# Optimization experiments

Hardware: AMD Instinct MI355X
Metric: run time of the kernel (lower is better)

## Reference

```python
import jax, jax.numpy as jnp
import numpy as np

N_NODES = 50000
N_EDGES = 600000
D = 128          # in = hidden = out (forced by residual adds)
HEADS = 4
HEAD_DIM = D // HEADS
EPS = 1e-5
NEG_SLOPE = 0.2  # PyG GATConv default


def setup_inputs() -> dict:
    key = jax.random.key(0)
    ks = jax.random.split(key, 12)
    s = 1.0 / np.sqrt(D)
    x = jax.random.normal(ks[0], (N_NODES, D), dtype=jnp.float32)
    edge_index = jax.random.randint(ks[1], (2, N_EDGES), 0, N_NODES, dtype=jnp.int32)
    # conv1: GATConv(D, D//heads, heads=heads)
    W1 = jax.random.normal(ks[2], (D, D), dtype=jnp.float32) * s
    a_src1 = jax.random.normal(ks[3], (HEADS, HEAD_DIM), dtype=jnp.float32) * s
    a_dst1 = jax.random.normal(ks[4], (HEADS, HEAD_DIM), dtype=jnp.float32) * s
    b1 = jnp.zeros((D,), dtype=jnp.float32)
    # conv2: GATConv(D, D, heads=1)
    W2 = jax.random.normal(ks[5], (D, D), dtype=jnp.float32) * s
    a_src2 = jax.random.normal(ks[6], (1, D), dtype=jnp.float32) * s
    a_dst2 = jax.random.normal(ks[7], (1, D), dtype=jnp.float32) * s
    b2 = jnp.zeros((D,), dtype=jnp.float32)
    # shared AddAndNorm BatchNorm1d params (same module used twice)
    bn_gamma = jnp.ones((D,), dtype=jnp.float32)
    bn_beta = jnp.zeros((D,), dtype=jnp.float32)
    return {"x": x, "edge_index": edge_index,
            "W1": W1, "a_src1": a_src1, "a_dst1": a_dst1, "b1": b1,
            "W2": W2, "a_src2": a_src2, "a_dst2": a_dst2, "b2": b2,
            "bn_gamma": bn_gamma, "bn_beta": bn_beta}


def _gat_conv(x, W, a_src, a_dst, b, src, dst, heads, head_dim):
    n = x.shape[0]
    h = (x @ W).reshape(n, heads, head_dim)                 # [N,H,C]
    e_src = jnp.einsum('nhc,hc->nh', h, a_src)              # [N,H]
    e_dst = jnp.einsum('nhc,hc->nh', h, a_dst)
    e = jax.nn.leaky_relu(e_src[src] + e_dst[dst], NEG_SLOPE)  # [E,H]
    # segment softmax over incoming edges per destination node
    m = jax.ops.segment_max(e, dst, num_segments=n)
    alpha = jnp.exp(e - m[dst])
    denom = jax.ops.segment_sum(alpha, dst, num_segments=n)
    alpha = alpha / denom[dst]
    out = jax.ops.segment_sum(alpha[:, :, None] * h[src], dst, num_segments=n)
    return out.reshape(n, heads * head_dim) + b


def _batch_norm(x, gamma, beta):
    mean = jnp.mean(x, axis=0)
    var = jnp.var(x, axis=0)
    return (x - mean) * jax.lax.rsqrt(var + EPS) * gamma + beta


def reference(x, edge_index, W1, a_src1, a_dst1, b1, W2, a_src2, a_dst2, b2,
              bn_gamma, bn_beta):
    n = x.shape[0]
    # PyG GATConv adds self loops by default
    loops = jnp.arange(n, dtype=edge_index.dtype)
    src = jnp.concatenate([edge_index[0], loops])
    dst = jnp.concatenate([edge_index[1], loops])

    res = x
    h = _gat_conv(x, W1, a_src1, a_dst1, b1, src, dst, HEADS, HEAD_DIM)
    h = _batch_norm(h + res, bn_gamma, bn_beta)   # dropout is identity (eval)
    h = jax.nn.relu(h)
    res = h
    h = _gat_conv(h, W2, a_src2, a_dst2, b2, src, dst, 1, D)
    h = _batch_norm(h + res, bn_gamma, bn_beta)
    return h
```

## Files before the change

kernel.cpp:

```cpp
#include <hip/hip_runtime.h>
#include <math.h>

#define NN 50000
#define NE 600000
#define ET (NE + NN)
#define D 128
#define EPSB 1e-5f
#define SLOPE 0.2f
#define XPITCH 136
#define SCB 196

typedef float f32x4 __attribute__((ext_vector_type(4)));
typedef short bf16x8 __attribute__((ext_vector_type(8)));

__device__ inline unsigned short bf16r(float f) {
    unsigned int u = __float_as_uint(f);
    unsigned int r = (u + 0x7fff + ((u >> 16) & 1)) >> 16;
    return (unsigned short)r;
}
__device__ inline float bflo(unsigned int u) { return __uint_as_float(u << 16); }
__device__ inline float bfhi(unsigned int u) { return __uint_as_float(u & 0xffff0000u); }

__global__ void hist_kernel(const int* __restrict__ ei, int* __restrict__ deg) {
    int e = blockIdx.x * blockDim.x + threadIdx.x;
    if (e >= ET) return;
    int dst = (e < NE) ? ei[NE + e] : (e - NE);
    atomicAdd(&deg[dst], 1);
}

__global__ __launch_bounds__(256) void scan_a_kernel(const int* __restrict__ deg,
                                                     int* __restrict__ tmp,
                                                     int* __restrict__ bsum) {
    __shared__ int sm[256];
    int t = threadIdx.x;
    int idx = blockIdx.x * 256 + t;
    int v = (idx < NN) ? deg[idx] : 0;
    sm[t] = v;
    __syncthreads();
    #pragma unroll
    for (int d = 1; d < 256; d <<= 1) {
        int add = (t >= d) ? sm[t - d] : 0;
        __syncthreads();
        sm[t] += add;
        __syncthreads();
    }
    if (idx < NN) tmp[idx] = sm[t];
    if (t == 255) bsum[blockIdx.x] = sm[255];
}

__global__ __launch_bounds__(256) void scan_b_kernel(const int* __restrict__ deg,
                                                     const int* __restrict__ tmp,
                                                     const int* __restrict__ bsum,
                                                     int* __restrict__ offs,
                                                     int* __restrict__ cur) {
    __shared__ int sm[256];
    int t = threadIdx.x;
    sm[t] = (t < SCB) ? bsum[t] : 0;
    __syncthreads();
    #pragma unroll
    for (int d = 1; d < 256; d <<= 1) {
        int add = (t >= d) ? sm[t - d] : 0;
        __syncthreads();
        sm[t] += add;
        __syncthreads();
    }
    int bpre = (blockIdx.x == 0) ? 0 : sm[blockIdx.x - 1];
    int idx = blockIdx.x * 256 + t;
    if (idx < NN) {
        int excl = bpre + tmp[idx] - deg[idx];
        offs[idx] = excl;
        cur[idx] = excl;
        if (idx == NN - 1) offs[NN] = bpre + tmp[idx];
    }
}

__global__ void scatter_kernel(const int* __restrict__ ei, int* __restrict__ cur,
                               int* __restrict__ ssrc) {
    int e = blockIdx.x * blockDim.x + threadIdx.x;
    if (e >= ET) return;
    int src, dst;
    if (e < NE) { src = ei[e]; dst = ei[NE + e]; }
    else        { src = dst = e - NE; }
    int pos = atomicAdd(&cur[dst], 1);
    ssrc[pos] = src;
}

__global__ void wconv_kernel(const float* __restrict__ W1, const float* __restrict__ W2,
                             unsigned short* __restrict__ wt1, unsigned short* __restrict__ wt2) {
    int t = blockIdx.x * blockDim.x + threadIdx.x;
    if (t >= 2 * D * D) return;
    int i = (t < D * D) ? t : t - D * D;
    int n = i >> 7, k = i & 127;
    if (t < D * D) wt1[i] = bf16r(W1[k * D + n]);
    else           wt2[i] = bf16r(W2[k * D + n]);
}

__global__ __launch_bounds__(256) void gemm_mfma_kernel(const float* __restrict__ X,
                                                        const unsigned short* __restrict__ Wt,
                                                        unsigned short* __restrict__ Hb, int nrows) {
    __shared__ unsigned short Xl[64 * XPITCH];
    __shared__ unsigned short Wl[128 * XPITCH];
    int t = threadIdx.x;
    int row0 = blockIdx.x * 64;

    {
        int r = t >> 1, cb = (t & 1) * 64;
        const uint4* src = (const uint4*)&Wt[r * D + cb];
        uint4* dst = (uint4*)&Wl[r * XPITCH + cb];
        #pragma unroll
        for (int j = 0; j < 8; ++j) dst[j] = src[j];
    }
    {
        int r = t >> 2, cb = (t & 3) * 32;
        int gr = row0 + r; if (gr >= nrows) gr = nrows - 1;
        const float4* src = (const float4*)&X[(long)gr * D + cb];
        #pragma unroll
        for (int j = 0; j < 8; ++j) {
            float4 v = src[j];
            ushort4 p;
            p.x = bf16r(v.x); p.y = bf16r(v.y);
            p.z = bf16r(v.z); p.w = bf16r(v.w);
            *(ushort4*)&Xl[r * XPITCH + cb + j * 4] = p;
        }
    }
    __syncthreads();

    int wv = t >> 6, l = t & 63;
    int lr = l & 15, lg = l >> 4;
    f32x4 acc[8];
    #pragma unroll
    for (int n = 0; n < 8; ++n) acc[n] = (f32x4){0.f, 0.f, 0.f, 0.f};

    #pragma unroll
    for (int kc = 0; kc < 4; ++kc) {
        bf16x8 a = *(const bf16x8*)&Xl[(wv * 16 + lr) * XPITCH + kc * 32 + lg * 8];
        #pragma unroll
        for (int n = 0; n < 8; ++n) {
            bf16x8 b = *(const bf16x8*)&Wl[(n * 16 + lr) * XPITCH + kc * 32 + lg * 8];
            acc[n] = __builtin_amdgcn_mfma_f32_16x16x32_bf16(a, b, acc[n], 0, 0, 0);
        }
    }
    int growb = row0 + wv * 16 + lg * 4;
    #pragma unroll
    for (int n = 0; n < 8; ++n) {
        #pragma unroll
        for (int j = 0; j < 4; ++j) {
            int gr = growb + j;
            if (gr < nrows) Hb[(long)gr * D + n * 16 + lr] = bf16r(acc[n][j]);
        }
    }
}

template <int H>
__global__ void logits_kernel(const unsigned short* __restrict__ Hb,
                              const float* __restrict__ a_src,
                              const float* __restrict__ a_dst,
                              float* __restrict__ es, float* __restrict__ ed) {
    int i = blockIdx.x * blockDim.x + threadIdx.x;
    if (i >= NN * H) return;
    int n = i / H, h = i % H;
    const int CH = D / H;
    const unsigned short* hp = Hb + (long)n * D + h * CH;
    const float* as = a_src + h * CH;
    const float* ad = a_dst + h * CH;
    float s = 0.f, d = 0.f;
    for (int c = 0; c < CH; c += 8) {
        uint4 u = *(const uint4*)&hp[c];
        float4 a0 = *(const float4*)&as[c];
        float4 a1 = *(const float4*)&as[c + 4];
        float4 b0 = *(const float4*)&ad[c];
        float4 b1 = *(const float4*)&ad[c + 4];
        float f0 = bflo(u.x), f1 = bfhi(u.x), f2 = bflo(u.y), f3 = bfhi(u.y);
        float f4 = bflo(u.z), f5 = bfhi(u.z), f6 = bflo(u.w), f7 = bfhi(u.w);
        s += f0 * a0.x + f1 * a0.y + f2 * a0.z + f3 * a0.w
           + f4 * a1.x + f5 * a1.y + f6 * a1.z + f7 * a1.w;
        d += f0 * b0.x + f1 * b0.y + f2 * b0.z + f3 * b0.w
           + f4 * b1.x + f5 * b1.y + f6 * b1.z + f7 * b1.w;
    }
    es[i] = s; ed[i] = d;
}

template <int H>
__global__ __launch_bounds__(256) void agg_kernel(const unsigned short* __restrict__ Hb,
                                                  const float* __restrict__ es,
                                                  const float* __restrict__ ed,
                                                  const int* __restrict__ offs,
                                                  const int* __restrict__ ssrc,
                                                  const float* __restrict__ bias,
                                                  const float* __restrict__ resid,
                                                  float* __restrict__ out) {
    int wave = threadIdx.x >> 6;
    int lane = threadIdx.x & 63;
    int dst = blockIdx.x * 4 + wave;
    if (dst >= NN) return;
    int h = (H == 1) ? 0 : (lane >> 4);
    int fo = lane * 2;
    float edv = ed[dst * H + h];
    int beg = offs[dst], end = offs[dst + 1];
    float2 a0 = {0.f,0.f}, a1 = {0.f,0.f}, a2 = {0.f,0.f}, a3 = {0.f,0.f};
    float d0 = 0.f, d1 = 0.f, d2 = 0.f, d3 = 0.f;
    int idx = beg;
    for (; idx + 3 < end; idx += 4) {
        int s0 = ssrc[idx], s1 = ssrc[idx+1], s2 = ssrc[idx+2], s3 = ssrc[idx+3];
        unsigned int u0 = *(const unsigned int*)&Hb[(long)s0 * D + fo];
        unsigned int u1 = *(const unsigned int*)&Hb[(long)s1 * D + fo];
        unsigned int u2 = *(const unsigned int*)&Hb[(long)s2 * D + fo];
        unsigned int u3 = *(const unsigned int*)&Hb[(long)s3 * D + fo];
        float e0 = es[s0*H+h] + edv; e0 = (e0 > 0.f) ? e0 : SLOPE*e0; float w0 = __expf(e0);
        float e1 = es[s1*H+h] + edv; e1 = (e1 > 0.f) ? e1 : SLOPE*e1; float w1 = __expf(e1);
        float e2 = es[s2*H+h] + edv; e2 = (e2 > 0.f) ? e2 : SLOPE*e2; float w2 = __expf(e2);
        float e3 = es[s3*H+h] + edv; e3 = (e3 > 0.f) ? e3 : SLOPE*e3; float w3 = __expf(e3);
        a0.x += w0 * bflo(u0); a0.y += w0 * bfhi(u0); d0 += w0;
        a1.x += w1 * bflo(u1); a1.y += w1 * bfhi(u1); d1 += w1;
        a2.x += w2 * bflo(u2); a2.y += w2 * bfhi(u2); d2 += w2;
        a3.x += w3 * bflo(u3); a3.y += w3 * bfhi(u3); d3 += w3;
    }
    for (; idx < end; ++idx) {
        int s0 = ssrc[idx];
        unsigned int u0 = *(const unsigned int*)&Hb[(long)s0 * D + fo];
        float e0 = es[s0*H+h] + edv; e0 = (e0 > 0.f) ? e0 : SLOPE*e0; float w0 = __expf(e0);
        a0.x += w0 * bflo(u0); a0.y += w0 * bfhi(u0); d0 += w0;
    }
    float dsum = (d0 + d1) + (d2 + d3);
    float accx = (a0.x + a1.x) + (a2.x + a3.x);
    float accy = (a0.y + a1.y) + (a2.y + a3.y);
    float inv = 1.0f / dsum;
    float2 r = *(const float2*)&resid[(long)dst * D + fo];
    float2 o;
    o.x = accx * inv + bias[fo]     + r.x;
    o.y = accy * inv + bias[fo + 1] + r.y;
    *(float2*)&out[(long)dst * D + fo] = o;
}

__global__ __launch_bounds__(128) void stats_kernel(const float* __restrict__ y,
                                                    float* __restrict__ st) {
    int f = threadIdx.x;
    float s = 0.f, q = 0.f;
    for (int r = blockIdx.x; r < NN; r += gridDim.x) {
        float v = y[(long)r * D + f];
        s += v; q += v * v;
    }
    atomicAdd(&st[f], s);
    atomicAdd(&st[D + f], q);
}

template <bool RELU>
__global__ __launch_bounds__(256) void apply_kernel(const float* __restrict__ y,
                                                    const float* __restrict__ st,
                                                    const float* __restrict__ gamma,
                                                    const float* __restrict__ beta,
                                                    float* __restrict__ out) {
    long i = (long)(blockIdx.x * blockDim.x + threadIdx.x) * 4;
    if (i >= (long)NN * D) return;
    int f = (int)(i & (D - 1));
    const float invn = 1.0f / NN;
    float4 sv = *(const float4*)&st[f];
    float4 qv = *(const float4*)&st[D + f];
    float4 gv = *(const float4*)&gamma[f];
    float4 bv = *(const float4*)&beta[f];
    float4 v = *(const float4*)&y[i];
    float4 o;
    float m, vr, g;
    m = sv.x * invn; vr = qv.x * invn - m * m; g = gv.x * rsqrtf(vr + EPSB);
    o.x = (v.x - m) * g + bv.x;
    m = sv.y * invn; vr = qv.y * invn - m * m; g = gv.y * rsqrtf(vr + EPSB);
    o.y = (v.y - m) * g + bv.y;
    m = sv.z * invn; vr = qv.z * invn - m * m; g = gv.z * rsqrtf(vr + EPSB);
    o.z = (v.z - m) * g + bv.z;
    m = sv.w * invn; vr = qv.w * invn - m * m; g = gv.w * rsqrtf(vr + EPSB);
    o.w = (v.w - m) * g + bv.w;
    if (RELU) {
        o.x = fmaxf(o.x, 0.f); o.y = fmaxf(o.y, 0.f);
        o.z = fmaxf(o.z, 0.f); o.w = fmaxf(o.w, 0.f);
    }
    *(float4*)&out[i] = o;
}

extern "C" void kernel_launch(void* const* d_in, const int* in_sizes, int n_in,
                              void* d_out, int out_size, void* d_ws, size_t ws_size,
                              hipStream_t stream) {
    const float* x      = (const float*)d_in[0];
    const int*   ei     = (const int*)  d_in[1];
    const float* W1     = (const float*)d_in[2];
    const float* a_src1 = (const float*)d_in[3];
    const float* a_dst1 = (const float*)d_in[4];
    const float* b1     = (const float*)d_in[5];
    const float* W2     = (const float*)d_in[6];
    const float* a_src2 = (const float*)d_in[7];
    const float* a_dst2 = (const float*)d_in[8];
    const float* b2     = (const float*)d_in[9];
    const float* gamma  = (const float*)d_in[10];
    const float* beta   = (const float*)d_in[11];
    float* out = (float*)d_out;

    unsigned short* Hb = (unsigned short*)d_ws;
    float* B    = (float*)d_ws + 3200000;
    float* Cres = B + 6400000;
    float* es1  = Cres + 6400000;
    float* ed1  = es1 + 200000;
    float* es2  = ed1 + 200000;
    float* ed2  = es2 + 50000;
    float* st1  = ed2 + 50000;
    float* st2  = st1 + 256;
    int*   deg  = (int*)(st2 + 256);
    int*   offs = deg + NN;
    int*   cur  = offs + NN + 1;
    int*   ssrc = cur + NN;
    int*   tmp  = ssrc + ET;
    int*   bsum = tmp + NN;
    unsigned short* wt1 = (unsigned short*)(bsum + SCB + 4);
    unsigned short* wt2 = wt1 + D * D;

    hipMemsetAsync(deg, 0, NN * sizeof(int), stream);
    hipMemsetAsync(st1, 0, 512 * sizeof(float), stream);

    wconv_kernel<<<(2 * D * D + 255) / 256, 256, 0, stream>>>(W1, W2, wt1, wt2);
    hist_kernel<<<(ET + 255) / 256, 256, 0, stream>>>(ei, deg);
    scan_a_kernel<<<SCB, 256, 0, stream>>>(deg, tmp, bsum);
    scan_b_kernel<<<SCB, 256, 0, stream>>>(deg, tmp, bsum, offs, cur);
    scatter_kernel<<<(ET + 255) / 256, 256, 0, stream>>>(ei, cur, ssrc);

    const int GG = (NN + 63) / 64;
    gemm_mfma_kernel<<<GG, 256, 0, stream>>>(x, wt1, Hb, NN);
    logits_kernel<4><<<(NN * 4 + 255) / 256, 256, 0, stream>>>(Hb, a_src1, a_dst1, es1, ed1);
    agg_kernel<4><<<(NN + 3) / 4, 256, 0, stream>>>(Hb, es1, ed1, offs, ssrc, b1, x, B);
    stats_kernel<<<1024, 128, 0, stream>>>(B, st1);
    apply_kernel<true><<<(NN * D / 4 + 255) / 256, 256, 0, stream>>>(B, st1, gamma, beta, Cres);

    gemm_mfma_kernel<<<GG, 256, 0, stream>>>(Cres, wt2, Hb, NN);
    logits_kernel<1><<<(NN + 255) / 256, 256, 0, stream>>>(Hb, a_src2, a_dst2, es2, ed2);
    agg_kernel<1><<<(NN + 3) / 4, 256, 0, stream>>>(Hb, es2, ed2, offs, ssrc, b2, Cres, out);
    stats_kernel<<<1024, 128, 0, stream>>>(out, st2);
    apply_kernel<false><<<(NN * D / 4 + 255) / 256, 256, 0, stream>>>(out, st2, gamma, beta, out);
}
```

Baseline: 375.3 us.

## Fuse first BatchNorm+ReLU into GEMM and aggregation, precompute edge weights

Removes the first apply_kernel and the Cres buffer. A finalize kernel computes per-feature scale and shift, which are then applied on the fly in the second GEMM's load and in the second aggregation's residual. Edge attention weights are now computed in a separate per-edge kernel using a new sorted-dst array, so the aggregation loop reads precomputed weights instead of gathering logits and computing exp per lane. This adds extra passes over edges and extra writes for sdst and wext, in exchange for less redundant exp work and one fewer full-tensor pass.

```diff
diff --git a/kernel.cpp b/kernel.cpp
--- a/kernel.cpp
+++ b/kernel.cpp
@@ -20,6 +20,7 @@
 }
 __device__ inline float bflo(unsigned int u) { return __uint_as_float(u << 16); }
 __device__ inline float bfhi(unsigned int u) { return __uint_as_float(u & 0xffff0000u); }
+__device__ inline float lrelu(float e) { return (e > 0.f) ? e : SLOPE * e; }
 
 __global__ void hist_kernel(const int* __restrict__ ei, int* __restrict__ deg) {
     int e = blockIdx.x * blockDim.x + threadIdx.x;
@@ -75,7 +76,7 @@
 }
 
 __global__ void scatter_kernel(const int* __restrict__ ei, int* __restrict__ cur,
-                               int* __restrict__ ssrc) {
+                               int* __restrict__ ssrc, int* __restrict__ sdst) {
     int e = blockIdx.x * blockDim.x + threadIdx.x;
     if (e >= ET) return;
     int src, dst;
@@ -83,6 +84,7 @@
     else        { src = dst = e - NE; }
     int pos = atomicAdd(&cur[dst], 1);
     ssrc[pos] = src;
+    sdst[pos] = dst;
 }
 
 __global__ void wconv_kernel(const float* __restrict__ W1, const float* __restrict__ W2,
@@ -95,8 +97,10 @@
     else           wt2[i] = bf16r(W2[k * D + n]);
 }
 
+template <bool BNRELU>
 __global__ __launch_bounds__(256) void gemm_mfma_kernel(const float* __restrict__ X,
                                                         const unsigned short* __restrict__ Wt,
+                                                        const float* __restrict__ scsh,
                                                         unsigned short* __restrict__ Hb, int nrows) {
     __shared__ unsigned short Xl[64 * XPITCH];
     __shared__ unsigned short Wl[128 * XPITCH];
@@ -117,6 +121,14 @@
         #pragma unroll
         for (int j = 0; j < 8; ++j) {
             float4 v = src[j];
+            if (BNRELU) {
+                float4 g = *(const float4*)&scsh[cb + j * 4];
+                float4 s = *(const float4*)&scsh[D + cb + j * 4];
+                v.x = fmaxf(fmaf(v.x, g.x, s.x), 0.f);
+                v.y = fmaxf(fmaf(v.y, g.y, s.y), 0.f);
+                v.z = fmaxf(fmaf(v.z, g.z, s.z), 0.f);
+                v.w = fmaxf(fmaf(v.w, g.w, s.w), 0.f);
+            }
             ushort4 p;
             p.x = bf16r(v.x); p.y = bf16r(v.y);
             p.z = bf16r(v.z); p.w = bf16r(v.w);
@@ -181,13 +193,34 @@
 }
 
 template <int H>
+__global__ void ew_kernel(const int* __restrict__ ssrc, const int* __restrict__ sdst,
+                          const float* __restrict__ es, const float* __restrict__ ed,
+                          float* __restrict__ wext) {
+    int i = blockIdx.x * blockDim.x + threadIdx.x;
+    if (i >= ET) return;
+    int s = ssrc[i], dd = sdst[i];
+    if (H == 4) {
+        float4 a = *(const float4*)&es[s * 4];
+        float4 b = *(const float4*)&ed[dd * 4];
+        float4 w;
+        w.x = __expf(lrelu(a.x + b.x));
+        w.y = __expf(lrelu(a.y + b.y));
+        w.z = __expf(lrelu(a.z + b.z));
+        w.w = __expf(lrelu(a.w + b.w));
+        *(float4*)&wext[i * 4] = w;
+    } else {
+        wext[i] = __expf(lrelu(es[s] + ed[dd]));
+    }
+}
+
+template <int H, bool RECON>
 __global__ __launch_bounds__(256) void agg_kernel(const unsigned short* __restrict__ Hb,
-                                                  const float* __restrict__ es,
-                                                  const float* __restrict__ ed,
+                                                  const float* __restrict__ wext,
                                                   const int* __restrict__ offs,
                                                   const int* __restrict__ ssrc,
                                                   const float* __restrict__ bias,
                                                   const float* __restrict__ resid,
+                                                  const float* __restrict__ scsh,
                                                   float* __restrict__ out) {
     int wave = threadIdx.x >> 6;
     int lane = threadIdx.x & 63;
@@ -195,21 +228,20 @@
     if (dst >= NN) return;
     int h = (H == 1) ? 0 : (lane >> 4);
     int fo = lane * 2;
-    float edv = ed[dst * H + h];
     int beg = offs[dst], end = offs[dst + 1];
     float2 a0 = {0.f,0.f}, a1 = {0.f,0.f}, a2 = {0.f,0.f}, a3 = {0.f,0.f};
     float d0 = 0.f, d1 = 0.f, d2 = 0.f, d3 = 0.f;
     int idx = beg;
     for (; idx + 3 < end; idx += 4) {
         int s0 = ssrc[idx], s1 = ssrc[idx+1], s2 = ssrc[idx+2], s3 = ssrc[idx+3];
+        float w0 = wext[(idx)   * H + h];
+        float w1 = wext[(idx+1) * H + h];
+        float w2 = wext[(idx+2) * H + h];
+        float w3 = wext[(idx+3) * H + h];
         unsigned int u0 = *(const unsigned int*)&Hb[(long)s0 * D + fo];
         unsigned int u1 = *(const unsigned int*)&Hb[(long)s1 * D + fo];
         unsigned int u2 = *(const unsigned int*)&Hb[(long)s2 * D + fo];
         unsigned int u3 = *(const unsigned int*)&Hb[(long)s3 * D + fo];
-        float e0 = es[s0*H+h] + edv; e0 = (e0 > 0.f) ? e0 : SLOPE*e0; float w0 = __expf(e0);
-        float e1 = es[s1*H+h] + edv; e1 = (e1 > 0.f) ? e1 : SLOPE*e1; float w1 = __expf(e1);
-        float e2 = es[s2*H+h] + edv; e2 = (e2 > 0.f) ? e2 : SLOPE*e2; float w2 = __expf(e2);
-        float e3 = es[s3*H+h] + edv; e3 = (e3 > 0.f) ? e3 : SLOPE*e3; float w3 = __expf(e3);
         a0.x += w0 * bflo(u0); a0.y += w0 * bfhi(u0); d0 += w0;
         a1.x += w1 * bflo(u1); a1.y += w1 * bfhi(u1); d1 += w1;
         a2.x += w2 * bflo(u2); a2.y += w2 * bfhi(u2); d2 += w2;
@@ -217,18 +249,24 @@
     }
     for (; idx < end; ++idx) {
         int s0 = ssrc[idx];
+        float w0 = wext[idx * H + h];
         unsigned int u0 = *(const unsigned int*)&Hb[(long)s0 * D + fo];
-        float e0 = es[s0*H+h] + edv; e0 = (e0 > 0.f) ? e0 : SLOPE*e0; float w0 = __expf(e0);
         a0.x += w0 * bflo(u0); a0.y += w0 * bfhi(u0); d0 += w0;
     }
     float dsum = (d0 + d1) + (d2 + d3);
     float accx = (a0.x + a1.x) + (a2.x + a3.x);
     float accy = (a0.y + a1.y) + (a2.y + a3.y);
     float inv = 1.0f / dsum;
-    float2 r = *(const float2*)&resid[(long)dst * D + fo];
+    float2 rr = *(const float2*)&resid[(long)dst * D + fo];
+    if (RECON) {
+        float2 g = *(const float2*)&scsh[fo];
+        float2 s = *(const float2*)&scsh[D + fo];
+        rr.x = fmaxf(fmaf(rr.x, g.x, s.x), 0.f);
+        rr.y = fmaxf(fmaf(rr.y, g.y, s.y), 0.f);
+    }
     float2 o;
-    o.x = accx * inv + bias[fo]     + r.x;
-    o.y = accy * inv + bias[fo + 1] + r.y;
+    o.x = accx * inv + bias[fo]     + rr.x;
+    o.y = accy * inv + bias[fo + 1] + rr.y;
     *(float2*)&out[(long)dst * D + fo] = o;
 }
 
@@ -242,6 +280,19 @@
     }
     atomicAdd(&st[f], s);
     atomicAdd(&st[D + f], q);
+}
+
+__global__ void finalize_kernel(const float* __restrict__ st,
+                                const float* __restrict__ gamma,
+                                const float* __restrict__ beta,
+                                float* __restrict__ scsh) {
+    int f = threadIdx.x;
+    if (f >= D) return;
+    float mean = st[f] * (1.0f / NN);
+    float var = st[D + f] * (1.0f / NN) - mean * mean;
+    float g = gamma[f] * rsqrtf(var + EPSB);
+    scsh[f] = g;
+    scsh[D + f] = beta[f] - mean * g;
 }
 
 template <bool RELU>
@@ -295,18 +346,20 @@
 
     unsigned short* Hb = (unsigned short*)d_ws;
     float* B    = (float*)d_ws + 3200000;
-    float* Cres = B + 6400000;
-    float* es1  = Cres + 6400000;
+    float* es1  = B + 6400000;
     float* ed1  = es1 + 200000;
     float* es2  = ed1 + 200000;
     float* ed2  = es2 + 50000;
     float* st1  = ed2 + 50000;
     float* st2  = st1 + 256;
-    int*   deg  = (int*)(st2 + 256);
+    float* scsh1= st2 + 256;
+    float* wext = scsh1 + 256;
+    int*   deg  = (int*)(wext + ET * 4);
     int*   offs = deg + NN;
     int*   cur  = offs + NN + 1;
     int*   ssrc = cur + NN;
-    int*   tmp  = ssrc + ET;
+    int*   sdst = ssrc + ET;
+    int*   tmp  = sdst + ET;
     int*   bsum = tmp + NN;
     unsigned short* wt1 = (unsigned short*)(bsum + SCB + 4);
     unsigned short* wt2 = wt1 + D * D;
@@ -318,18 +371,21 @@
     hist_kernel<<<(ET + 255) / 256, 256, 0, stream>>>(ei, deg);
     scan_a_kernel<<<SCB, 256, 0, stream>>>(deg, tmp, bsum);
     scan_b_kernel<<<SCB, 256, 0, stream>>>(deg, tmp, bsum, offs, cur);
-    scatter_kernel<<<(ET + 255) / 256, 256, 0, stream>>>(ei, cur, ssrc);
+    scatter_kernel<<<(ET + 255) / 256, 256, 0, stream>>>(ei, cur, ssrc, sdst);
 
     const int GG = (NN + 63) / 64;
-    gemm_mfma_kernel<<<GG, 256, 0, stream>>>(x, wt1, Hb, NN);
+    const int EB = (ET + 255) / 256;
+    gemm_mfma_kernel<false><<<GG, 256, 0, stream>>>(x, wt1, nullptr, Hb, NN);
     logits_kernel<4><<<(NN * 4 + 255) / 256, 256, 0, stream>>>(Hb, a_src1, a_dst1, es1, ed1);
-    agg_kernel<4><<<(NN + 3) / 4, 256, 0, stream>>>(Hb, es1, ed1, offs, ssrc, b1, x, B);
+    ew_kernel<4><<<EB, 256, 0, stream>>>(ssrc, sdst, es1, ed1, wext);
+    agg_kernel<4, false><<<(NN + 3) / 4, 256, 0, stream>>>(Hb, wext, offs, ssrc, b1, x, nullptr, B);
     stats_kernel<<<1024, 128, 0, stream>>>(B, st1);
-    apply_kernel<true><<<(NN * D / 4 + 255) / 256, 256, 0, stream>>>(B, st1, gamma, beta, Cres);
-
-    gemm_mfma_kernel<<<GG, 256, 0, stream>>>(Cres, wt2, Hb, NN);
+    finalize_kernel<<<1, 128, 0, stream>>>(st1, gamma, beta, scsh1);
+
+    gemm_mfma_kernel<true><<<GG, 256, 0, stream>>>(B, wt2, scsh1, Hb, NN);
     logits_kernel<1><<<(NN + 255) / 256, 256, 0, stream>>>(Hb, a_src2, a_dst2, es2, ed2);
-    agg_kernel<1><<<(NN + 3) / 4, 256, 0, stream>>>(Hb, es2, ed2, offs, ssrc, b2, Cres, out);
+    ew_kernel<1><<<EB, 256, 0, stream>>>(ssrc, sdst, es2, ed2, wext);
+    agg_kernel<1, true><<<(NN + 3) / 4, 256, 0, stream>>>(Hb, wext, offs, ssrc, b2, B, scsh1, out);
     stats_kernel<<<1024, 128, 0, stream>>>(out, st2);
     apply_kernel<false><<<(NN * D / 4 + 255) / 256, 256, 0, stream>>>(out, st2, gamma, beta, out);
 }
```

Result: slower. 383.5 us (+2.2%).
